# Kernel tuning notes

Measured on AMD Instinct MI355X. Metric: run time of the kernel, lower is better.

The kernel has to match this reference:

```python
import jax, jax.numpy as jnp
import numpy as np

N = 50000      # nodes (spots)
E = 800000     # edges (avg degree 16)
G = 1002       # num_genes + 2
D = 256        # latent_dim
C = 20         # num_celltypes
BN_EPS = 1e-5


def setup_inputs() -> dict:
    key = jax.random.key(0)
    ks = jax.random.split(key, 14)
    def p(k, shape, fan_in):
        return (jax.random.normal(k, shape, jnp.float32) / np.sqrt(fan_in)).astype(jnp.float32)
    return {
        "x": jax.random.normal(ks[0], (N, G), jnp.float32),
        "edge_index": jax.random.randint(ks[1], (2, E), 0, N, jnp.int64),
        "lin_w": p(ks[2], (G, D), G),          # encoder Linear (no bias)
        "conv1_w": p(ks[3], (D, D), D),
        "conv1_b": jnp.zeros((D,), jnp.float32),
        "conv2_w": p(ks[4], (D, D), D),
        "conv2_b": jnp.zeros((D,), jnp.float32),
        "mlp1_w": p(ks[5], (D, D), D),
        "mlp1_b": jnp.zeros((D,), jnp.float32),
        "bn_gamma": jnp.ones((D,), jnp.float32),
        "bn_beta": jnp.zeros((D,), jnp.float32),
        "mlp2_w": p(ks[6], (D, C), D),
        "mlp2_b": jnp.zeros((C,), jnp.float32),
    }


def _gcn_conv(x, src, dst, W, b):
    # x: [N, D]; symmetric GCN normalization with self-loops (weight 1)
    n = x.shape[0]
    x = x @ W
    deg = jax.ops.segment_sum(jnp.ones(src.shape[0], x.dtype), dst, num_segments=n) + 1.0
    dinv = jax.lax.rsqrt(deg)
    norm = dinv[src] * dinv[dst]                 # [E]
    agg = jax.ops.segment_sum(norm[:, None] * x[src], dst, num_segments=n)
    agg = agg + x * (1.0 / deg)[:, None]         # self-loop term: deg^-1 * x_i
    return agg + b


def reference(x, edge_index, lin_w, conv1_w, conv1_b, conv2_w, conv2_b,
              mlp1_w, mlp1_b, bn_gamma, bn_beta, mlp2_w, mlp2_b):
    src, dst = edge_index[0], edge_index[1]
    # encoder
    h = x @ lin_w
    h = jax.nn.relu(_gcn_conv(h, src, dst, conv1_w, conv1_b))
    h = jax.nn.relu(_gcn_conv(h, src, dst, conv2_w, conv2_b))
    # decoder MLP (Linear -> BatchNorm(train) -> ReLU -> Linear) + softmax
    h = h @ mlp1_w + mlp1_b
    mu = jnp.mean(h, axis=0)
    var = jnp.var(h, axis=0)
    h = (h - mu) * jax.lax.rsqrt(var + BN_EPS) * bn_gamma + bn_beta
    h = jax.nn.relu(h)
    h = h @ mlp2_w + mlp2_b
    return jax.nn.softmax(h, axis=-1)
```

## Files before the change

### kernel.cpp

```cpp
#include <hip/hip_runtime.h>
#include <cstdint>
#include <cstddef>

typedef unsigned short u16;
typedef unsigned int   u32;
typedef _Float16       f16;
typedef u16  u16x4 __attribute__((ext_vector_type(4)));
typedef u16  u16x8 __attribute__((ext_vector_type(8)));
typedef f16  f16x8 __attribute__((ext_vector_type(8)));
typedef float f32x4 __attribute__((ext_vector_type(4)));

static __device__ __forceinline__ u16 f2h(float f){
  f16 h = (f16)f;
  return __builtin_bit_cast(u16, h);
}
static __device__ __forceinline__ float h2f(u16 b){
  f16 h = __builtin_bit_cast(f16, b);
  return (float)h;
}

static __device__ __forceinline__ void async16(void* lds, const void* g){
  __builtin_amdgcn_global_load_lds(
      (const __attribute__((address_space(1))) u32*)g,
      (__attribute__((address_space(3))) u32*)lds, 16, 0, 0);
}

__global__ void transpose_weights(const float* __restrict__ lw, const float* __restrict__ w1,
                                  const float* __restrict__ w2, const float* __restrict__ w3,
                                  u16* __restrict__ lwT, u16* __restrict__ w1T,
                                  u16* __restrict__ w2T, u16* __restrict__ w3T,
                                  int G, int Gpad)
{
  __shared__ float t[32][33];
  int z = blockIdx.z;
  const float* in = (z==0)? lw : (z==1)? w1 : (z==2)? w2 : w3;
  u16* out        = (z==0)? lwT: (z==1)? w1T: (z==2)? w2T: w3T;
  int R   = (z==0)? G : 256;
  int ldo = (z==0)? Gpad : 256;
  int by = blockIdx.y, bx = blockIdx.x;
  if (by*32 >= R && z != 0) return;
  int tid = threadIdx.x;
  #pragma unroll
  for (int k=0;k<4;k++){
    int p = tid + k*256; int r = p>>5, c = p&31;
    int gr = by*32 + r;
    t[r][c] = (gr < R) ? in[gr*256 + bx*32 + c] : 0.f;
  }
  __syncthreads();
  #pragma unroll
  for (int k=0;k<4;k++){
    int p = tid + k*256; int r = p>>5, c = p&31;
    int oc = by*32 + c;
    if (oc < ldo) out[(bx*32 + r)*ldo + oc] = f2h(t[c][r]);
  }
}

__global__ __launch_bounds__(256) void pack_x(
    const float* __restrict__ x, u16* __restrict__ P, int N, int G)
{
  int tid = threadIdx.x;
  int r   = blockIdx.x*8 + (tid>>5);
  int c8l = tid & 31;
  int m = r >> 7, R = r & 127, q = R >> 4, rr = R & 15;
  int sc = (rr >> 1) & 3;
  bool rv = r < N;
  const float* xr = x + (size_t)r*G;
  #pragma unroll
  for (int p=0;p<4;p++){
    int c8 = c8l + p*32;
    int c0 = c8*8;
    u16x8 o;
    #pragma unroll
    for (int j=0;j<8;j+=2){
      float2 v = {0.f, 0.f};
      if (rv && (c0 + j + 1) < G)      v = *(const float2*)(xr + c0 + j);
      else if (rv && (c0 + j) < G)     v.x = xr[c0 + j];
      o[j]   = f2h(v.x);
      o[j+1] = f2h(v.y);
    }
    int t  = c8 >> 2;
    int gg = c8 & 3;
    int ss = gg ^ sc;
    int l  = rr*4 + ss;
    *(u16x8*)(P + ((size_t)(m*32 + t))*4096 + q*512 + l*8) = o;
  }
}

__global__ void count_kernel(const int* __restrict__ dst, int* __restrict__ cnt, int E){
  int e = blockIdx.x*256 + threadIdx.x;
  if (e < E) atomicAdd(&cnt[dst[e]], 1);
}

__global__ void scan_reduce(const int* __restrict__ cnt, int* __restrict__ bsum, int N){
  __shared__ int s[256];
  int tid = threadIdx.x;
  int i = blockIdx.x*256 + tid;
  s[tid] = (i<N)? cnt[i] : 0;
  __syncthreads();
  for (int off=128; off>0; off>>=1){
    if (tid < off) s[tid] += s[tid+off];
    __syncthreads();
  }
  if (tid==0) bsum[blockIdx.x] = s[0];
}

__global__ void scan_offsets(const int* __restrict__ bsum, int* __restrict__ boff, int nb){
  __shared__ int s[256];
  int tid = threadIdx.x;
  int v = (tid<nb)? bsum[tid] : 0;
  s[tid] = v; __syncthreads();
  for (int off=1; off<256; off<<=1){
    int t = (tid>=off)? s[tid-off] : 0;
    __syncthreads();
    s[tid] += t;
    __syncthreads();
  }
  if (tid<nb) boff[tid] = s[tid]-v;
}

__global__ void scan_final(const int* __restrict__ cnt, const int* __restrict__ boff,
                           int* __restrict__ row_ptr, float* __restrict__ dinv, int N, int E){
  __shared__ int s[256];
  int tid = threadIdx.x;
  int i = blockIdx.x*256 + tid;
  int v = (i<N)? cnt[i] : 0;
  s[tid] = v; __syncthreads();
  for (int off=1; off<256; off<<=1){
    int t = (tid>=off)? s[tid-off] : 0;
    __syncthreads();
    s[tid] += t;
    __syncthreads();
  }
  if (i < N){
    row_ptr[i] = boff[blockIdx.x] + s[tid] - v;
    dinv[i] = rsqrtf((float)(v+1));
  }
  if (i == N-1) row_ptr[N] = E;
}

__global__ void scatter_kernel(const int* __restrict__ src, const int* __restrict__ dst,
                               const int* __restrict__ row_ptr, int* __restrict__ cursor,
                               int* __restrict__ colx, int E){
  int e = blockIdx.x*256 + threadIdx.x;
  if (e < E){
    int d = dst[e];
    int pos = atomicAdd(&cursor[d], 1);
    colx[row_ptr[d] + pos] = src[e];
  }
}

template<bool APACKED, bool ADD_BIAS>
__global__ __launch_bounds__(256) void gemm_async(
    const u16* __restrict__ Ah, int lda,
    const u16* __restrict__ BT, int Kpad,
    u16* __restrict__ C, const float* __restrict__ bias, int M)
{
  __shared__ __align__(16) u16 As[2][4096];
  __shared__ __align__(16) u16 Bs[2][4096];

  const int tid  = threadIdx.x;
  const int lane = tid & 63;
  const int quad = lane >> 4;
  const int l16  = lane & 15;
  const int wave = tid >> 6;
  const int wm = (wave >> 1) << 6;
  const int wn = (wave & 1) << 6;
  const int m0 = blockIdx.y << 7;
  const int n0 = blockIdx.x << 7;

  const u16* bg[2];
  u16* lB[2];
  #pragma unroll
  for (int i=0;i<2;i++){
    int q = wave*2 + i;
    int rr = lane >> 2, ss = lane & 3;
    int gg = ss ^ ((rr >> 1) & 3);
    bg[i] = BT + (size_t)(n0 + q*16 + rr)*Kpad + gg*8;
    lB[i] = &Bs[0][0] + q*512;
  }

  const u16* ag[2];
  u16* lA[2];
  #pragma unroll
  for (int i=0;i<2;i++){
    int q = wave*2 + i;
    if constexpr (APACKED){
      ag[i] = Ah + (size_t)blockIdx.y*32*4096 + q*512 + lane*8;
    } else {
      int rr = lane >> 2, ss = lane & 3;
      int gg = ss ^ ((rr >> 1) & 3);
      int gr = m0 + q*16 + rr;
      if (gr >= M) gr = M-1;
      ag[i] = Ah + (size_t)gr*lda + gg*8;
    }
    lA[i] = &As[0][0] + q*512;
  }

  auto stage = [&](int buf, int t){
    const int kb = t << 5;
    #pragma unroll
    for (int i=0;i<2;i++) async16(lB[i] + buf*4096, bg[i] + kb);
    #pragma unroll
    for (int i=0;i<2;i++)
      async16(lA[i] + buf*4096, APACKED ? (ag[i] + (size_t)t*4096) : (ag[i] + kb));
  };

  f32x4 acc[4][4];
  #pragma unroll
  for (int i=0;i<4;i++)
    #pragma unroll
    for (int j=0;j<4;j++) acc[i][j] = {0.f,0.f,0.f,0.f};

  const int NT = Kpad >> 5;

  stage(0, 0);
  int cur = 0;
  for (int t=0; t<NT; ++t){
    if (t+1 < NT){
      stage(cur^1, t+1);
      asm volatile("s_waitcnt vmcnt(4)" ::: "memory");
    } else {
      asm volatile("s_waitcnt vmcnt(0)" ::: "memory");
    }
    __builtin_amdgcn_s_barrier();

    const u16* AshC = &As[cur][0];
    const u16* BsC  = &Bs[cur][0];

    f16x8 af[4], bf[4];
    #pragma unroll
    for (int mt=0;mt<4;mt++){
      int R = wm + mt*16 + l16;
      int s = quad ^ ((R >> 1) & 3);
      af[mt] = __builtin_bit_cast(f16x8, *(const u16x8*)(AshC + R*32 + s*8));
    }
    #pragma unroll
    for (int nt=0;nt<4;nt++){
      int R = wn + nt*16 + l16;
      int s = quad ^ ((R >> 1) & 3);
      bf[nt] = __builtin_bit_cast(f16x8, *(const u16x8*)(BsC + R*32 + s*8));
    }
    #pragma unroll
    for (int mt=0;mt<4;mt++)
      #pragma unroll
      for (int nt=0;nt<4;nt++)
        acc[mt][nt] = __builtin_amdgcn_mfma_f32_16x16x32_f16(af[mt], bf[nt], acc[mt][nt], 0, 0, 0);

    __builtin_amdgcn_s_barrier();
    cur ^= 1;
  }

  #pragma unroll
  for (int mt=0;mt<4;mt++){
    #pragma unroll
    for (int nt=0;nt<4;nt++){
      int col = n0 + wn + nt*16 + l16;
      float bv = 0.f;
      if constexpr (ADD_BIAS) bv = bias[col];
      #pragma unroll
      for (int r=0;r<4;r++){
        int row = m0 + wm + mt*16 + quad*4 + r;
        if (row < M) C[(size_t)row*256 + col] = f2h(acc[mt][nt][r] + bv);
      }
    }
  }
}

__global__ __launch_bounds__(256) void agg_kernel(
    const u16* __restrict__ XW, const float* __restrict__ bias,
    const float* __restrict__ dinv, const int* __restrict__ row_ptr,
    const int* __restrict__ colx, u16* __restrict__ H, int N)
{
  int wid = (blockIdx.x << 2) + (threadIdx.x >> 6);
  if (wid >= N) return;
  int lane = threadIdx.x & 63;
  int f = lane << 2;
  float di = dinv[wid];
  int e0 = row_ptr[wid], e1 = row_ptr[wid+1];
  int deg = e1 - e0;
  float a0=0.f, a1=0.f, a2=0.f, a3=0.f;
  for (int base = 0; base < deg; base += 64){
    int mi = 0;
    if (base + lane < deg) mi = colx[e0 + base + lane];
    int cnt = min(deg - base, 64);
    int j = 0;
    for (; j+1 < cnt; j += 2){
      int s0 = __shfl(mi, j);
      int s1 = __shfl(mi, j+1);
      float w0 = dinv[s0]*di;
      float w1 = dinv[s1]*di;
      u16x4 x0 = *(const u16x4*)(XW + (size_t)s0*256 + f);
      u16x4 x1 = *(const u16x4*)(XW + (size_t)s1*256 + f);
      a0 += w0*h2f(x0[0]) + w1*h2f(x1[0]);
      a1 += w0*h2f(x0[1]) + w1*h2f(x1[1]);
      a2 += w0*h2f(x0[2]) + w1*h2f(x1[2]);
      a3 += w0*h2f(x0[3]) + w1*h2f(x1[3]);
    }
    if (j < cnt){
      int s0 = __shfl(mi, j);
      float w0 = dinv[s0]*di;
      u16x4 x0 = *(const u16x4*)(XW + (size_t)s0*256 + f);
      a0 += w0*h2f(x0[0]); a1 += w0*h2f(x0[1]);
      a2 += w0*h2f(x0[2]); a3 += w0*h2f(x0[3]);
    }
  }
  u16x4 xs = *(const u16x4*)(XW + (size_t)wid*256 + f);
  float wd = di*di;
  a0 += wd*h2f(xs[0]); a1 += wd*h2f(xs[1]); a2 += wd*h2f(xs[2]); a3 += wd*h2f(xs[3]);
  const float4 bb = *(const float4*)(bias + f);
  a0 = fmaxf(a0 + bb.x, 0.f);
  a1 = fmaxf(a1 + bb.y, 0.f);
  a2 = fmaxf(a2 + bb.z, 0.f);
  a3 = fmaxf(a3 + bb.w, 0.f);
  u16x4 o = { f2h(a0), f2h(a1), f2h(a2), f2h(a3) };
  *(u16x4*)(H + (size_t)wid*256 + f) = o;
}

__global__ void bn_stats(const u16* __restrict__ H, float* __restrict__ bsum,
                         float* __restrict__ bsq, int N){
  int col = threadIdx.x;
  float s=0.f, q=0.f;
  for (int r=blockIdx.x; r<N; r+=gridDim.x){
    float v = h2f(H[(size_t)r*256 + col]);
    s += v; q += v*v;
  }
  atomicAdd(&bsum[col], s);
  atomicAdd(&bsq[col], q);
}

__global__ void bn_finalize(const float* __restrict__ bsum, const float* __restrict__ bsq,
                            const float* __restrict__ gamma, const float* __restrict__ beta,
                            float* __restrict__ scale, float* __restrict__ shift, int N){
  int c = threadIdx.x;
  float invN = 1.f/(float)N;
  float mu  = bsum[c]*invN;
  float var = bsq[c]*invN - mu*mu;
  float sc  = gamma[c] * rsqrtf(var + 1e-5f);
  scale[c] = sc;
  shift[c] = beta[c] - mu*sc;
}

__global__ __launch_bounds__(256) void final_kernel(
    const u16* __restrict__ H, const float* __restrict__ scale, const float* __restrict__ shift,
    const float* __restrict__ W2, const float* __restrict__ b2, float* __restrict__ out, int N)
{
  __shared__ float W2s[256*20];
  __shared__ float scs[256];
  __shared__ float shs[256];
  __shared__ float b2s[20];
  int tid = threadIdx.x;
  for (int i=tid; i<5120; i+=256) W2s[i] = W2[i];
  scs[tid] = scale[tid];
  shs[tid] = shift[tid];
  if (tid < 20) b2s[tid] = b2[tid];
  __syncthreads();
  int r = blockIdx.x*256 + tid;
  if (r >= N) return;
  float l[20];
  #pragma unroll
  for (int c=0;c<20;c++) l[c] = b2s[c];
  const u16* hrow = H + (size_t)r*256;
  for (int j0=0;j0<256;j0+=8){
    u16x8 h8 = *(const u16x8*)(hrow + j0);
    #pragma unroll
    for (int t=0;t<8;t++){
      int j = j0+t;
      float a = fmaxf(fmaf(h2f(h8[t]), scs[j], shs[j]), 0.f);
      const float* wr = W2s + j*20;
      #pragma unroll
      for (int c=0;c<20;c++) l[c] = fmaf(a, wr[c], l[c]);
    }
  }
  float m = l[0];
  #pragma unroll
  for (int c=1;c<20;c++) m = fmaxf(m, l[c]);
  float ssum = 0.f;
  #pragma unroll
  for (int c=0;c<20;c++){ l[c] = __expf(l[c]-m); ssum += l[c]; }
  float inv = 1.f/ssum;
  float* orow = out + (size_t)r*20;
  #pragma unroll
  for (int c=0;c<20;c++) orow[c] = l[c]*inv;
}

extern "C" void kernel_launch(void* const* d_in, const int* in_sizes, int n_in,
                              void* d_out, int out_size, void* d_ws, size_t ws_size,
                              hipStream_t stream)
{
  (void)n_in; (void)out_size; (void)ws_size;
  const float* x     = (const float*)d_in[0];
  const int*   ei    = (const int*)d_in[1];
  const float* lin_w = (const float*)d_in[2];
  const float* c1w   = (const float*)d_in[3];
  const float* c1b   = (const float*)d_in[4];
  const float* c2w   = (const float*)d_in[5];
  const float* c2b   = (const float*)d_in[6];
  const float* m1w   = (const float*)d_in[7];
  const float* m1b   = (const float*)d_in[8];
  const float* gam   = (const float*)d_in[9];
  const float* bet   = (const float*)d_in[10];
  const float* m2w   = (const float*)d_in[11];
  const float* m2b   = (const float*)d_in[12];
  float* out = (float*)d_out;

  const int E = in_sizes[1]/2;
  const int G = in_sizes[2]/256;
  const int N = in_sizes[0]/G;
  const int Gpad = (G + 31) & ~31;
  const int MB128 = (N + 127) >> 7;
  const int* srcI = ei;
  const int* dstI = ei + E;

  char* w = (char*)d_ws;
  auto alloc = [&](size_t bytes)->char*{
    char* p = w;
    w += (bytes + 255) & ~(size_t)255;
    return p;
  };
  u16* Ha    = (u16*)alloc((size_t)N*256*2);
  u16* Hb    = (u16*)alloc((size_t)N*256*2);
  u16* packA = (u16*)alloc((size_t)MB128*128*Gpad*2);
  u16* linT  = (u16*)alloc((size_t)256*Gpad*2);
  u16* w1T   = (u16*)alloc(256*256*2);
  u16* w2T   = (u16*)alloc(256*256*2);
  u16* w3T   = (u16*)alloc(256*256*2);
  int* cnt    = (int*)alloc((size_t)N*4);
  int* cursor = (int*)alloc((size_t)N*4);
  int* rowp   = (int*)alloc((size_t)(N+1)*4);
  int* colx   = (int*)alloc((size_t)E*4);
  float* dinv = (float*)alloc((size_t)N*4);
  int* bsum   = (int*)alloc(1024);
  int* boff   = (int*)alloc(1024);
  float* bnsum= (float*)alloc(1024);
  float* bnsq = (float*)alloc(1024);
  float* scl  = (float*)alloc(1024);
  float* shf  = (float*)alloc(1024);

  hipMemsetAsync(cnt,    0, (size_t)N*4, stream);
  hipMemsetAsync(cursor, 0, (size_t)N*4, stream);
  hipMemsetAsync(bnsum,  0, 2048, stream);

  const int NB = (N + 255)/256;

  transpose_weights<<<dim3(8, Gpad>>5, 4), 256, 0, stream>>>(
      lin_w, c1w, c2w, m1w, linT, w1T, w2T, w3T, G, Gpad);
  pack_x<<<dim3(MB128*16), 256, 0, stream>>>(x, packA, N, G);
  count_kernel  <<<dim3((E+255)/256), 256, 0, stream>>>(dstI, cnt, E);
  scan_reduce   <<<dim3(NB), 256, 0, stream>>>(cnt, bsum, N);
  scan_offsets  <<<dim3(1),  256, 0, stream>>>(bsum, boff, NB);
  scan_final    <<<dim3(NB), 256, 0, stream>>>(cnt, boff, rowp, dinv, N, E);
  scatter_kernel<<<dim3((E+255)/256), 256, 0, stream>>>(srcI, dstI, rowp, cursor, colx, E);

  dim3 ggrid(2, MB128);
  gemm_async<true,  false><<<ggrid, 256, 0, stream>>>(packA, 0,  linT, Gpad, Ha, nullptr, N);
  gemm_async<false, false><<<ggrid, 256, 0, stream>>>(Ha, 256, w1T,  256,  Hb, nullptr, N);
  agg_kernel<<<dim3((N+3)/4), 256, 0, stream>>>(Hb, c1b, dinv, rowp, colx, Ha, N);
  gemm_async<false, false><<<ggrid, 256, 0, stream>>>(Ha, 256, w2T,  256,  Hb, nullptr, N);
  agg_kernel<<<dim3((N+3)/4), 256, 0, stream>>>(Hb, c2b, dinv, rowp, colx, Ha, N);
  gemm_async<false, true ><<<ggrid, 256, 0, stream>>>(Ha, 256, w3T,  256,  Hb, m1b, N);
  bn_stats   <<<dim3(256), 256, 0, stream>>>(Hb, bnsum, bnsq, N);
  bn_finalize<<<dim3(1),   256, 0, stream>>>(bnsum, bnsq, gam, bet, scl, shf, N);
  final_kernel<<<dim3(NB), 256, 0, stream>>>(Hb, scl, shf, m2w, m2b, out, N);
}
```

Before: 752.4 us.

## Replace LDS-staged GEMM with register-direct single-wave GEMM on pre-packed fragment layouts

Replaces the 256-thread, LDS double-buffered GEMM with a 64-thread kernel that loads MFMA fragments directly from global memory into registers. This works because weights, inputs and aggregation outputs are now written in a pre-packed tile layout that matches the fragments. The goal is to remove LDS traffic, barriers and swizzle arithmetic, and to raise the block count to 64x64 tiles for better occupancy across CUs. The cost is that every wave fetches its operand tiles from global/L2 with no sharing through LDS, so the same data is reloaded more often. It also adds scattered writes in the packed layouts produced by agg_kernel and the first GEMM.

Result: slower. 779.0 us (+3.5%).

```diff
diff --git a/kernel.cpp b/kernel.cpp
--- a/kernel.cpp
+++ b/kernel.cpp
@@ -19,24 +19,20 @@
   return (float)h;
 }
 
-static __device__ __forceinline__ void async16(void* lds, const void* g){
-  __builtin_amdgcn_global_load_lds(
-      (const __attribute__((address_space(1))) u32*)g,
-      (__attribute__((address_space(3))) u32*)lds, 16, 0, 0);
-}
 
 __global__ void transpose_weights(const float* __restrict__ lw, const float* __restrict__ w1,
                                   const float* __restrict__ w2, const float* __restrict__ w3,
-                                  u16* __restrict__ lwT, u16* __restrict__ w1T,
-                                  u16* __restrict__ w2T, u16* __restrict__ w3T,
+                                  u16* __restrict__ lwP, u16* __restrict__ w1P,
+                                  u16* __restrict__ w2P, u16* __restrict__ w3P,
                                   int G, int Gpad)
 {
   __shared__ float t[32][33];
   int z = blockIdx.z;
   const float* in = (z==0)? lw : (z==1)? w1 : (z==2)? w2 : w3;
-  u16* out        = (z==0)? lwT: (z==1)? w1T: (z==2)? w2T: w3T;
+  u16* out        = (z==0)? lwP: (z==1)? w1P: (z==2)? w2P: w3P;
   int R   = (z==0)? G : 256;
   int ldo = (z==0)? Gpad : 256;
+  int NTz = ldo >> 5;
   int by = blockIdx.y, bx = blockIdx.x;
   if (by*32 >= R && z != 0) return;
   int tid = threadIdx.x;
@@ -50,8 +46,13 @@
   #pragma unroll
   for (int k=0;k<4;k++){
     int p = tid + k*256; int r = p>>5, c = p&31;
-    int oc = by*32 + c;
-    if (oc < ldo) out[(bx*32 + r)*ldo + oc] = f2h(t[c][r]);
+    int n  = bx*32 + r;
+    int kk = by*32 + c;
+    if (kk < ldo){
+      int idx = ((n>>6)*NTz + (kk>>5))*2048 + ((n>>4)&3)*512
+              + ((n&15)*4 + ((kk>>3)&3))*8 + (kk&7);
+      out[idx] = f2h(t[c][r]);
+    }
   }
 }
 
@@ -62,7 +63,6 @@
   int r   = blockIdx.x*8 + (tid>>5);
   int c8l = tid & 31;
   int m = r >> 7, R = r & 127, q = R >> 4, rr = R & 15;
-  int sc = (rr >> 1) & 3;
   bool rv = r < N;
   const float* xr = x + (size_t)r*G;
   #pragma unroll
@@ -80,8 +80,7 @@
     }
     int t  = c8 >> 2;
     int gg = c8 & 3;
-    int ss = gg ^ sc;
-    int l  = rr*4 + ss;
+    int l  = rr*4 + gg;
     *(u16x8*)(P + ((size_t)(m*32 + t))*4096 + q*512 + l*8) = o;
   }
 }
@@ -149,118 +148,91 @@
   }
 }
 
-template<bool APACKED, bool ADD_BIAS>
-__global__ __launch_bounds__(256) void gemm_async(
-    const u16* __restrict__ Ah, int lda,
-    const u16* __restrict__ BT, int Kpad,
-    u16* __restrict__ C, const float* __restrict__ bias, int M)
-{
-  __shared__ __align__(16) u16 As[2][4096];
-  __shared__ __align__(16) u16 Bs[2][4096];
-
-  const int tid  = threadIdx.x;
-  const int lane = tid & 63;
+template<int ASTRIDE, bool CPACK, bool ADD_BIAS>
+__global__ __launch_bounds__(64) void gemm64(
+    const u16* __restrict__ A, const u16* __restrict__ B,
+    u16* __restrict__ C, const float* __restrict__ bias, int M, int NT)
+{
+  const int lane = threadIdx.x & 63;
   const int quad = lane >> 4;
   const int l16  = lane & 15;
-  const int wave = tid >> 6;
-  const int wm = (wave >> 1) << 6;
-  const int wn = (wave & 1) << 6;
-  const int m0 = blockIdx.y << 7;
-  const int n0 = blockIdx.x << 7;
-
-  const u16* bg[2];
-  u16* lB[2];
-  #pragma unroll
-  for (int i=0;i<2;i++){
-    int q = wave*2 + i;
-    int rr = lane >> 2, ss = lane & 3;
-    int gg = ss ^ ((rr >> 1) & 3);
-    bg[i] = BT + (size_t)(n0 + q*16 + rr)*Kpad + gg*8;
-    lB[i] = &Bs[0][0] + q*512;
-  }
-
-  const u16* ag[2];
-  u16* lA[2];
-  #pragma unroll
-  for (int i=0;i<2;i++){
-    int q = wave*2 + i;
-    if constexpr (APACKED){
-      ag[i] = Ah + (size_t)blockIdx.y*32*4096 + q*512 + lane*8;
-    } else {
-      int rr = lane >> 2, ss = lane & 3;
-      int gg = ss ^ ((rr >> 1) & 3);
-      int gr = m0 + q*16 + rr;
-      if (gr >= M) gr = M-1;
-      ag[i] = Ah + (size_t)gr*lda + gg*8;
-    }
-    lA[i] = &As[0][0] + q*512;
-  }
-
-  auto stage = [&](int buf, int t){
-    const int kb = t << 5;
-    #pragma unroll
-    for (int i=0;i<2;i++) async16(lB[i] + buf*4096, bg[i] + kb);
-    #pragma unroll
-    for (int i=0;i<2;i++)
-      async16(lA[i] + buf*4096, APACKED ? (ag[i] + (size_t)t*4096) : (ag[i] + kb));
+  const int m64  = blockIdx.y;
+  const int nblk = blockIdx.x;
+  const int la   = (l16*4 + quad) * 8;
+
+  const u16* Ap = (ASTRIDE == 4096)
+      ? A + (size_t)(m64 >> 1) * NT * 4096 + (m64 & 1) * 2048 + la
+      : A + (size_t)m64 * NT * 2048 + la;
+  const u16* Bp = B + (size_t)nblk * NT * 2048 + la;
+
+  f32x4 acc[4][4];
+  #pragma unroll
+  for (int i=0;i<4;i++)
+    #pragma unroll
+    for (int j=0;j<4;j++) acc[i][j] = {0.f,0.f,0.f,0.f};
+
+  f16x8 a0[4], b0[4], a1[4], b1[4];
+
+  auto LD = [&](f16x8* fa, f16x8* fb){
+    #pragma unroll
+    for (int i=0;i<4;i++) fa[i] = *(const f16x8*)(Ap + i*512);
+    #pragma unroll
+    for (int i=0;i<4;i++) fb[i] = *(const f16x8*)(Bp + i*512);
+    Ap += ASTRIDE;
+    Bp += 2048;
   };
-
-  f32x4 acc[4][4];
-  #pragma unroll
-  for (int i=0;i<4;i++)
-    #pragma unroll
-    for (int j=0;j<4;j++) acc[i][j] = {0.f,0.f,0.f,0.f};
-
-  const int NT = Kpad >> 5;
-
-  stage(0, 0);
-  int cur = 0;
-  for (int t=0; t<NT; ++t){
-    if (t+1 < NT){
-      stage(cur^1, t+1);
-      asm volatile("s_waitcnt vmcnt(4)" ::: "memory");
-    } else {
-      asm volatile("s_waitcnt vmcnt(0)" ::: "memory");
-    }
-    __builtin_amdgcn_s_barrier();
-
-    const u16* AshC = &As[cur][0];
-    const u16* BsC  = &Bs[cur][0];
-
-    f16x8 af[4], bf[4];
-    #pragma unroll
-    for (int mt=0;mt<4;mt++){
-      int R = wm + mt*16 + l16;
-      int s = quad ^ ((R >> 1) & 3);
-      af[mt] = __builtin_bit_cast(f16x8, *(const u16x8*)(AshC + R*32 + s*8));
-    }
-    #pragma unroll
-    for (int nt=0;nt<4;nt++){
-      int R = wn + nt*16 + l16;
-      int s = quad ^ ((R >> 1) & 3);
-      bf[nt] = __builtin_bit_cast(f16x8, *(const u16x8*)(BsC + R*32 + s*8));
-    }
+  auto CP = [&](const f16x8* fa, const f16x8* fb){
     #pragma unroll
     for (int mt=0;mt<4;mt++)
       #pragma unroll
       for (int nt=0;nt<4;nt++)
-        acc[mt][nt] = __builtin_amdgcn_mfma_f32_16x16x32_f16(af[mt], bf[nt], acc[mt][nt], 0, 0, 0);
-
-    __builtin_amdgcn_s_barrier();
-    cur ^= 1;
-  }
-
-  #pragma unroll
-  for (int mt=0;mt<4;mt++){
-    #pragma unroll
-    for (int nt=0;nt<4;nt++){
-      int col = n0 + wn + nt*16 + l16;
-      float bv = 0.f;
-      if constexpr (ADD_BIAS) bv = bias[col];
+        acc[mt][nt] = __builtin_amdgcn_mfma_f32_16x16x32_f16(fa[mt], fb[nt], acc[mt][nt], 0, 0, 0);
+  };
+
+  LD(a0, b0);
+  for (int t=0; t+2 < NT; t+=2){
+    LD(a1, b1); CP(a0, b0);
+    LD(a0, b0); CP(a1, b1);
+  }
+  LD(a1, b1); CP(a0, b0); CP(a1, b1);
+
+  float bv[4];
+  if constexpr (ADD_BIAS){
+    #pragma unroll
+    for (int nt=0;nt<4;nt++) bv[nt] = bias[nblk*64 + nt*16 + l16];
+  }
+
+  if constexpr (CPACK){
+    #pragma unroll
+    for (int mt=0;mt<4;mt++){
       #pragma unroll
-      for (int r=0;r<4;r++){
-        int row = m0 + wm + mt*16 + quad*4 + r;
-        if (row < M) C[(size_t)row*256 + col] = f2h(acc[mt][nt][r] + bv);
+      for (int nt=0;nt<4;nt++){
+        int tcol = nblk*2 + (nt>>1);
+        int gg   = (nt*2 + (l16>>3)) & 3;
+        int e    = l16 & 7;
+        #pragma unroll
+        for (int r=0;r<4;r++){
+          int rr = quad*4 + r;
+          size_t idx = ((size_t)m64*8 + tcol)*2048 + mt*512 + (rr*4+gg)*8 + e;
+          float v = acc[mt][nt][r];
+          if constexpr (ADD_BIAS) v += bv[nt];
+          C[idx] = f2h(v);
+        }
+      }
+    }
+  } else {
+    #pragma unroll
+    for (int mt=0;mt<4;mt++){
+      #pragma unroll
+      for (int nt=0;nt<4;nt++){
+        int col = nblk*64 + nt*16 + l16;
+        #pragma unroll
+        for (int r=0;r<4;r++){
+          int row = m64*64 + mt*16 + quad*4 + r;
+          float v = acc[mt][nt][r];
+          if constexpr (ADD_BIAS) v += bv[nt];
+          if (row < M) C[(size_t)row*256 + col] = f2h(v);
+        }
       }
     }
   }
@@ -269,7 +241,7 @@
 __global__ __launch_bounds__(256) void agg_kernel(
     const u16* __restrict__ XW, const float* __restrict__ bias,
     const float* __restrict__ dinv, const int* __restrict__ row_ptr,
-    const int* __restrict__ colx, u16* __restrict__ H, int N)
+    const int* __restrict__ colx, u16* __restrict__ Hp, int N)
 {
   int wid = (blockIdx.x << 2) + (threadIdx.x >> 6);
   if (wid >= N) return;
@@ -313,7 +285,12 @@
   a2 = fmaxf(a2 + bb.z, 0.f);
   a3 = fmaxf(a3 + bb.w, 0.f);
   u16x4 o = { f2h(a0), f2h(a1), f2h(a2), f2h(a3) };
-  *(u16x4*)(H + (size_t)wid*256 + f) = o;
+  int t  = f >> 5;
+  int gg = (f >> 3) & 3;
+  int e  = f & 7;
+  int rr = wid & 15, q = (wid >> 4) & 3, m64 = wid >> 6;
+  size_t idx = ((size_t)m64*8 + t)*2048 + q*512 + (rr*4+gg)*8 + e;
+  *(u16x4*)(Hp + idx) = o;
 }
 
 __global__ void bn_stats(const u16* __restrict__ H, float* __restrict__ bsum,
@@ -408,6 +385,7 @@
   const int N = in_sizes[0]/G;
   const int Gpad = (G + 31) & ~31;
   const int MB128 = (N + 127) >> 7;
+  const int M64   = (N + 63) >> 6;
   const int* srcI = ei;
   const int* dstI = ei + E;
 
@@ -417,13 +395,13 @@
     w += (bytes + 255) & ~(size_t)255;
     return p;
   };
-  u16* Ha    = (u16*)alloc((size_t)N*256*2);
-  u16* Hb    = (u16*)alloc((size_t)N*256*2);
+  u16* Hpack = (u16*)alloc((size_t)M64*8*2048*2);
+  u16* Hrow  = (u16*)alloc((size_t)N*256*2);
   u16* packA = (u16*)alloc((size_t)MB128*128*Gpad*2);
-  u16* linT  = (u16*)alloc((size_t)256*Gpad*2);
-  u16* w1T   = (u16*)alloc(256*256*2);
-  u16* w2T   = (u16*)alloc(256*256*2);
-  u16* w3T   = (u16*)alloc(256*256*2);
+  u16* linP  = (u16*)alloc((size_t)4*(Gpad>>5)*2048*2);
+  u16* w1P   = (u16*)alloc((size_t)4*8*2048*2);
+  u16* w2P   = (u16*)alloc((size_t)4*8*2048*2);
+  u16* w3P   = (u16*)alloc((size_t)4*8*2048*2);
   int* cnt    = (int*)alloc((size_t)N*4);
   int* cursor = (int*)alloc((size_t)N*4);
   int* rowp   = (int*)alloc((size_t)(N+1)*4);
@@ -443,7 +421,7 @@
   const int NB = (N + 255)/256;
 
   transpose_weights<<<dim3(8, Gpad>>5, 4), 256, 0, stream>>>(
-      lin_w, c1w, c2w, m1w, linT, w1T, w2T, w3T, G, Gpad);
+      lin_w, c1w, c2w, m1w, linP, w1P, w2P, w3P, G, Gpad);
   pack_x<<<dim3(MB128*16), 256, 0, stream>>>(x, packA, N, G);
   count_kernel  <<<dim3((E+255)/256), 256, 0, stream>>>(dstI, cnt, E);
   scan_reduce   <<<dim3(NB), 256, 0, stream>>>(cnt, bsum, N);
@@ -451,14 +429,14 @@
   scan_final    <<<dim3(NB), 256, 0, stream>>>(cnt, boff, rowp, dinv, N, E);
   scatter_kernel<<<dim3((E+255)/256), 256, 0, stream>>>(srcI, dstI, rowp, cursor, colx, E);
 
-  dim3 ggrid(2, MB128);
-  gemm_async<true,  false><<<ggrid, 256, 0, stream>>>(packA, 0,  linT, Gpad, Ha, nullptr, N);
-  gemm_async<false, false><<<ggrid, 256, 0, stream>>>(Ha, 256, w1T,  256,  Hb, nullptr, N);
-  agg_kernel<<<dim3((N+3)/4), 256, 0, stream>>>(Hb, c1b, dinv, rowp, colx, Ha, N);
-  gemm_async<false, false><<<ggrid, 256, 0, stream>>>(Ha, 256, w2T,  256,  Hb, nullptr, N);
-  agg_kernel<<<dim3((N+3)/4), 256, 0, stream>>>(Hb, c2b, dinv, rowp, colx, Ha, N);
-  gemm_async<false, true ><<<ggrid, 256, 0, stream>>>(Ha, 256, w3T,  256,  Hb, m1b, N);
-  bn_stats   <<<dim3(256), 256, 0, stream>>>(Hb, bnsum, bnsq, N);
+  dim3 ggrid(4, M64);
+  gemm64<4096, true,  false><<<ggrid, 64, 0, stream>>>(packA, linP, Hpack, nullptr, N, Gpad>>5);
+  gemm64<2048, false, false><<<ggrid, 64, 0, stream>>>(Hpack, w1P, Hrow, nullptr, N, 8);
+  agg_kernel<<<dim3((N+3)/4), 256, 0, stream>>>(Hrow, c1b, dinv, rowp, colx, Hpack, N);
+  gemm64<2048, false, false><<<ggrid, 64, 0, stream>>>(Hpack, w2P, Hrow, nullptr, N, 8);
+  agg_kernel<<<dim3((N+3)/4), 256, 0, stream>>>(Hrow, c2b, dinv, rowp, colx, Hpack, N);
+  gemm64<2048, false, true ><<<ggrid, 64, 0, stream>>>(Hpack, w3P, Hrow, m1b, N, 8);
+  bn_stats   <<<dim3(256), 256, 0, stream>>>(Hrow, bnsum, bnsq, N);
   bn_finalize<<<dim3(1),   256, 0, stream>>>(bnsum, bnsq, gam, bet, scl, shf, N);
-  final_kernel<<<dim3(NB), 256, 0, stream>>>(Hb, scl, shf, m2w, m2b, out, N);
-}
+  final_kernel<<<dim3(NB), 256, 0, stream>>>(Hrow, scl, shf, m2w, m2b, out, N);
+}
```
